# Kernel tuning notes

Hardware: AMD Instinct MI355X
Metric: run time of the kernel (lower is better)

## Reference

```python
import jax, jax.numpy as jnp
import numpy as np

H = 32        # num heads
D = 80        # head dim
HID = 2560    # hidden size = H*D
ROT = 32      # rotary dim = int(0.4*80)
THETA = 10000.0
T = 2048      # total packed tokens
B = 4         # sequences
SEQ = 512     # tokens per sequence
CACHE = 4096  # paged cache slots


def setup_inputs() -> dict:
    key = jax.random.key(0)
    ks = jax.random.split(key, 10)
    bound = 1.0 / np.sqrt(HID)

    def lin(k):
        kw, kb = jax.random.split(k)
        W = jax.random.uniform(kw, (HID, HID), jnp.float32, -bound, bound)
        b = jax.random.uniform(kb, (HID,), jnp.float32, -bound, bound)
        return W, b

    Wq, bq = lin(ks[0])
    Wk, bk = lin(ks[1])
    Wv, bv = lin(ks[2])
    Wd, bd = lin(ks[3])
    h = jax.random.normal(ks[4], (T, HID), jnp.float32)
    return {
        "h": h,
        "k_cache": jnp.zeros((CACHE, HID), jnp.float32),
        "v_cache": jnp.zeros((CACHE, HID), jnp.float32),
        "positions": (jnp.arange(T) % SEQ).astype(jnp.int32),
        "offsets": (jnp.arange(B + 1) * SEQ).astype(jnp.int32),
        "cache_indices": jnp.arange(T, dtype=jnp.int32),
        "Wq": Wq, "bq": bq, "Wk": Wk, "bk": bk,
        "Wv": Wv, "bv": bv, "Wd": Wd, "bd": bd,
    }


def _rotate_half(x):
    x1, x2 = jnp.split(x, 2, axis=-1)
    return jnp.concatenate([-x2, x1], axis=-1)


def reference(h, k_cache, v_cache, positions, offsets, cache_indices,
              Wq, bq, Wk, bk, Wv, bv, Wd, bd):
    # QKV projections (torch Linear: x @ W.T + b)
    q = h @ Wq.T + bq
    k = h @ Wk.T + bk
    v = h @ Wv.T + bv

    q3 = q.reshape(T, H, D)
    k3 = k.reshape(T, H, D)

    # partial RoPE on first ROT dims of each head
    pos = positions.astype(jnp.float32)
    inv_freq = 1.0 / (THETA ** (jnp.arange(0, ROT, 2, dtype=jnp.float32) / ROT))
    freqs = pos[:, None] * inv_freq                      # [T, ROT/2]
    emb = jnp.concatenate([freqs, freqs], axis=-1)       # [T, ROT]
    cos = jnp.cos(emb)[:, None, :]                       # [T, 1, ROT]
    sin = jnp.sin(emb)[:, None, :]

    q_rot, q_pass = q3[..., :ROT], q3[..., ROT:]
    k_rot, k_pass = k3[..., :ROT], k3[..., ROT:]
    q_rot = q_rot * cos + _rotate_half(q_rot) * sin
    k_rot = k_rot * cos + _rotate_half(k_rot) * sin
    q3 = jnp.concatenate([q_rot, q_pass], axis=-1)
    k3 = jnp.concatenate([k_rot, k_pass], axis=-1)

    # prompt_init=True path: scatter rotated k and v into paged caches
    new_k_cache = k_cache.at[cache_indices].set(k3.reshape(T, HID))
    new_v_cache = v_cache.at[cache_indices].set(v)

    # variable-length causal attention over packed sequences
    scale = D ** -0.5
    scores = jnp.einsum('thd,shd->hts', q3, k3) * scale   # [H, T, T]
    idx = jnp.arange(T)
    seg = jnp.searchsorted(offsets[1:], idx, side='right')
    mask = (seg[:, None] == seg[None, :]) & (idx[:, None] >= idx[None, :])
    scores = jnp.where(mask[None], scores, jnp.float32(-1e30))
    p = jax.nn.softmax(scores, axis=-1)
    o = jnp.einsum('hts,shd->thd', p, v.reshape(T, H, D)).reshape(T, HID)

    out = o @ Wd.T + bd
    return out, new_k_cache, new_v_cache
```

## Files before the change

kernel.cpp:

```cpp
#include <hip/hip_runtime.h>
#include <cstdint>
#include <cstddef>


#define HIDDEN 2560
#define SEQT 2048
#define NHEADS 32
#define DHEAD 80
#define NSEG 4
#define SEGLEN 512
#define CACHE_ROWS 4096
#define QSCALE 0.11180339887498949f

typedef __bf16 bf16_8 __attribute__((ext_vector_type(8)));
typedef unsigned short u16x8 __attribute__((ext_vector_type(8)));
typedef float f32x4 __attribute__((ext_vector_type(4)));

__device__ __forceinline__ unsigned short f2bf(float f) {
  unsigned int u = __builtin_bit_cast(unsigned int, f);
  u += 0x7fffu + ((u >> 16) & 1u);
  return (unsigned short)(u >> 16);
}
__device__ __forceinline__ float bf2f(unsigned short s) {
  unsigned int u = ((unsigned int)s) << 16;
  return __builtin_bit_cast(float, u);
}

__device__ __forceinline__ void gload16(const unsigned short* g, unsigned short* l) {
  __builtin_amdgcn_global_load_lds(
      (const __attribute__((address_space(1))) unsigned int*)g,
      (__attribute__((address_space(3))) unsigned int*)l, 16, 0, 0);
}

#define BAR() asm volatile("s_barrier" ::: "memory")
#define LGKM0()                                          \
  do {                                                   \
    asm volatile("s_waitcnt lgkmcnt(0)" ::: "memory");   \
    __builtin_amdgcn_sched_barrier(0);                   \
  } while (0)
#define PRIO(x) __builtin_amdgcn_s_setprio(x)
#define MF(af, bf, c) c = __builtin_amdgcn_mfma_f32_16x16x32_bf16(af, bf, c, 0, 0, 0)

__global__ __launch_bounds__(256) void prep_kernel(
    const float* __restrict__ s0, const float* __restrict__ s1,
    const float* __restrict__ s2, const float* __restrict__ s3,
    const float* __restrict__ s4,
    const float* __restrict__ kci, const float* __restrict__ vci,
    unsigned short* __restrict__ d0, unsigned short* __restrict__ d1,
    unsigned short* __restrict__ d2, unsigned short* __restrict__ d3,
    unsigned short* __restrict__ d4,
    float* __restrict__ kco, float* __restrict__ vco) {
  const int z = blockIdx.z;
  const int stride = gridDim.x * blockDim.x;
  int i = blockIdx.x * blockDim.x + threadIdx.x;
  if (z < 5) {
    const float* s = z == 0 ? s0 : z == 1 ? s1 : z == 2 ? s2 : z == 3 ? s3 : s4;
    unsigned short* d = z == 0 ? d0 : z == 1 ? d1 : z == 2 ? d2 : z == 3 ? d3 : d4;
    const int n4 = (z < 4) ? (HIDDEN * HIDDEN / 4) : (SEQT * HIDDEN / 4);
    for (; i < n4; i += stride) {
      float4 v = ((const float4*)s)[i];
      ushort4 o;
      o.x = f2bf(v.x); o.y = f2bf(v.y); o.z = f2bf(v.z); o.w = f2bf(v.w);
      ((ushort4*)d)[i] = o;
    }
  } else {
    const int n4 = SEQT * HIDDEN / 4;
    const float4* s = (const float4*)(z == 5 ? kci : vci);
    float4* d = (float4*)(z == 5 ? kco : vco);
    for (; i < n4; i += stride) d[i + n4] = s[i + n4];
  }
}

template <int OUTMODE>
__device__ __forceinline__ void gemm256_body(
    const unsigned short* __restrict__ A, const unsigned short* __restrict__ Bg,
    const float* __restrict__ bias, void* __restrict__ C,
    int m0, int n0, int kbase, int nt) {
  constexpr int K = HIDDEN;
  __shared__ __align__(16) unsigned short L[65536];

  const int tid = threadIdx.x;
  const int lane = tid & 63;
  const int wid = tid >> 6;
  const int l15 = lane & 15;
  const int kg = lane >> 4;
  const int wm = wid >> 2;
  const int wn = wid & 3;

  const int g8 = (((tid & 7) - (tid >> 3)) & 7) * 8;
  const int srow = tid >> 3;
  const unsigned short* As0 = A + (size_t)(m0 + srow) * K + kbase + g8;
  const unsigned short* As1 = As0 + (size_t)128 * K;
  const unsigned short* Bs0 = Bg + (size_t)(n0 + srow) * K + kbase + g8;
  const unsigned short* Bs1 = Bs0 + (size_t)128 * K;
  const int t16 = tid * 8;

  auto stA0 = [&](int kt) {
    const int b = (kt & 1) * 32768, ko = kt * 64;
    gload16(As0 + ko, L + b + t16);
    gload16(As1 + ko, L + b + 8192 + t16);
  };
  auto stA1 = [&](int kt) {
    const int b = (kt & 1) * 32768, ko = 64 * K + kt * 64;
    gload16(As0 + ko, L + b + 4096 + t16);
    gload16(As1 + ko, L + b + 12288 + t16);
  };
  auto stB0 = [&](int kt) {
    const int b = (kt & 1) * 32768 + 16384, ko = kt * 64;
    gload16(Bs0 + ko, L + b + t16);
    gload16(Bs0 + 64 * K + ko, L + b + 4096 + t16);
  };
  auto stB1 = [&](int kt) {
    const int b = (kt & 1) * 32768 + 16384 + 8192, ko = kt * 64;
    gload16(Bs1 + ko, L + b + t16);
    gload16(Bs1 + 64 * K + ko, L + b + 4096 + t16);
  };

  const int c0 = (kg + l15) & 7;
  const int aof0 = wm * 8192 + l15 * 64 + c0 * 8;
  const int aof1 = wm * 8192 + l15 * 64 + (c0 ^ 4) * 8;
  const int bof0 = 16384 + wn * 4096 + l15 * 64 + c0 * 8;
  const int bof1 = 16384 + wn * 4096 + l15 * 64 + (c0 ^ 4) * 8;

  f32x4 acc[8][4];
#pragma unroll
  for (int m = 0; m < 8; m++)
#pragma unroll
    for (int n = 0; n < 4; n++) acc[m][n] = f32x4{0.f, 0.f, 0.f, 0.f};

  bf16_8 a[4][2], bl[2][2], bh[2][2];

#define DSR(off) (*(const bf16_8*)(L + (off)))
  auto rdA = [&](int off) {
#pragma unroll
    for (int fm = 0; fm < 4; fm++) {
      a[fm][0] = DSR(off + aof0 + fm * 1024);
      a[fm][1] = DSR(off + aof1 + fm * 1024);
    }
  };
  auto rdBl = [&](int off) {
#pragma unroll
    for (int fn = 0; fn < 2; fn++) {
      bl[fn][0] = DSR(off + bof0 + fn * 1024);
      bl[fn][1] = DSR(off + bof1 + fn * 1024);
    }
  };
  auto rdBh = [&](int off) {
#pragma unroll
    for (int fn = 0; fn < 2; fn++) {
      bh[fn][0] = DSR(off + bof0 + (2 + fn) * 1024);
      bh[fn][1] = DSR(off + bof1 + (2 + fn) * 1024);
    }
  };
  auto mmq = [&](int mq, int nq, bf16_8 (&bb)[2][2]) {
#pragma unroll
    for (int fm = 0; fm < 4; fm++)
#pragma unroll
      for (int fn = 0; fn < 2; fn++) {
        MF(a[fm][0], bb[fn][0], acc[mq * 4 + fm][nq * 2 + fn]);
        MF(a[fm][1], bb[fn][1], acc[mq * 4 + fm][nq * 2 + fn]);
      }
  };

  stA0(0); stB0(0); stB1(0); stA1(0);
  stA0(1); stB0(1); stB1(1);
  asm volatile("s_waitcnt vmcnt(6)" ::: "memory");
  BAR();

#pragma unroll 2
  for (int t = 0; t < nt - 2; ++t) {
    const int bo = (t & 1) * 32768;
    rdA(bo); rdBl(bo);
    stA1(t + 1);
    BAR(); LGKM0(); PRIO(1); mmq(0, 0, bl); PRIO(0); BAR();
    rdBh(bo);
    stA0(t + 2);
    BAR(); LGKM0(); PRIO(1); mmq(0, 1, bh); PRIO(0); BAR();
    rdA(bo + 4096);
    stB0(t + 2);
    BAR(); LGKM0(); PRIO(1); mmq(1, 0, bl); PRIO(0); BAR();
    stB1(t + 2);
    BAR(); PRIO(1); mmq(1, 1, bh); PRIO(0);
    asm volatile("s_waitcnt vmcnt(6)" ::: "memory");
    BAR();
  }

  {
    const int bo = 0;
    rdA(bo); rdBl(bo);
    stA1(nt - 1);
    BAR(); LGKM0(); PRIO(1); mmq(0, 0, bl); PRIO(0); BAR();
    rdBh(bo);
    BAR(); LGKM0(); PRIO(1); mmq(0, 1, bh); PRIO(0); BAR();
    rdA(bo + 4096);
    BAR(); LGKM0(); PRIO(1); mmq(1, 0, bl); PRIO(0); BAR();
    BAR(); PRIO(1); mmq(1, 1, bh); PRIO(0);
    asm volatile("s_waitcnt vmcnt(0)" ::: "memory");
    BAR();
  }
  {
    const int bo = 32768;
    rdA(bo); rdBl(bo);
    BAR(); LGKM0(); PRIO(1); mmq(0, 0, bl); PRIO(0); BAR();
    rdBh(bo);
    BAR(); LGKM0(); PRIO(1); mmq(0, 1, bh); PRIO(0); BAR();
    rdA(bo + 4096);
    BAR(); LGKM0(); PRIO(1); mmq(1, 0, bl); PRIO(0); BAR();
    PRIO(1); mmq(1, 1, bh); PRIO(0);
  }
#undef DSR

#pragma unroll
  for (int n4 = 0; n4 < 4; n4++) {
    const int col = n0 + wn * 64 + n4 * 16 + l15;
    const float bv = (OUTMODE == 2) ? 0.f : bias[col];
#pragma unroll
    for (int m8 = 0; m8 < 8; m8++) {
      const int rowb = m0 + wm * 128 + m8 * 16 + kg * 4;
#pragma unroll
      for (int j = 0; j < 4; j++) {
        float val = acc[m8][n4][j] + bv;
        if (OUTMODE == 0)
          ((unsigned short*)C)[(size_t)(rowb + j) * HIDDEN + col] = f2bf(val);
        else
          ((float*)C)[(size_t)(rowb + j) * HIDDEN + col] = val;
      }
    }
  }
}

__global__ __launch_bounds__(512, 2) void gemm_qkv8_kernel(
    const unsigned short* __restrict__ A,
    const unsigned short* __restrict__ B0, const unsigned short* __restrict__ B1,
    const unsigned short* __restrict__ B2,
    const float* __restrict__ bias0, const float* __restrict__ bias1,
    const float* __restrict__ bias2,
    unsigned short* __restrict__ C0, unsigned short* __restrict__ C1,
    unsigned short* __restrict__ C2) {
  const int lb = blockIdx.x + 8 * (blockIdx.y + 10 * blockIdx.z);
  const int swz = (lb & 7) * 30 + (lb >> 3);
  const int mx = swz & 7;
  const int r = swz >> 3;
  const int ny = r % 10;
  const int zz = r / 10;
  const unsigned short* B = zz == 0 ? B0 : (zz == 1 ? B1 : B2);
  const float* bias = zz == 0 ? bias0 : (zz == 1 ? bias1 : bias2);
  unsigned short* C = zz == 0 ? C0 : (zz == 1 ? C1 : C2);
  gemm256_body<0>(A, B, bias, C, mx * 256, ny * 256, 0, 40);
}

__global__ __launch_bounds__(512, 2) void gemm_out8_kernel(
    const unsigned short* __restrict__ A, const unsigned short* __restrict__ B,
    float* __restrict__ P0, float* __restrict__ P1, float* __restrict__ P2) {
  const int lb = blockIdx.x + 8 * (blockIdx.y + 10 * blockIdx.z);
  const int swz = (lb & 7) * 30 + (lb >> 3);
  const int mx = swz & 7;
  const int r = swz >> 3;
  const int ny = r % 10;
  const int kz = r / 10;
  float* P = kz == 0 ? P0 : (kz == 1 ? P1 : P2);
  const int kbase = kz * 896;
  const int nt = (kz == 2) ? 12 : 14;
  gemm256_body<2>(A, B, nullptr, P, mx * 256, ny * 256, kbase, nt);
}

__global__ __launch_bounds__(256) void reduce3_bias_kernel(
    const float* __restrict__ p0, const float* __restrict__ p1,
    const float* __restrict__ p2, const float* __restrict__ bias,
    float* __restrict__ out, int n4) {
  int i = blockIdx.x * blockDim.x + threadIdx.x;
  const int stride = gridDim.x * blockDim.x;
  for (; i < n4; i += stride) {
    float4 a = ((const float4*)p0)[i];
    float4 b = ((const float4*)p1)[i];
    float4 c = ((const float4*)p2)[i];
    const int cb = (i * 4) % HIDDEN;
    float4 bv = *(const float4*)&bias[cb];
    float4 o;
    o.x = a.x + b.x + c.x + bv.x;
    o.y = a.y + b.y + c.y + bv.y;
    o.z = a.z + b.z + c.z + bv.z;
    o.w = a.w + b.w + c.w + bv.w;
    ((float4*)out)[i] = o;
  }
}

__global__ __launch_bounds__(256) void rope_scatter_kernel(
    unsigned short* __restrict__ qb, unsigned short* __restrict__ kb,
    const unsigned short* __restrict__ vb,
    const int* __restrict__ positions, const int* __restrict__ cidx,
    float* __restrict__ kco, float* __restrict__ vco) {
  const int t = blockIdx.x;
  const int tid = threadIdx.x;
  __shared__ float cs[16], sn[16];

  if (tid < 16) {
    const float pos = (float)positions[t];
    const float inv = expf(-(float)tid * (9.210340371976184f / 16.0f));
    const float f = pos * inv;
    cs[tid] = cosf(f);
    sn[tid] = sinf(f);
  }
  __syncthreads();

  {
    unsigned short* buf = (tid >> 7) ? kb : qb;
    const int r = tid & 127;
    const int head = r >> 2;
    const int d0 = (r & 3) * 4;
    unsigned short* p = buf + (size_t)t * HIDDEN + head * DHEAD + d0;
    ushort4 u1 = *(const ushort4*)p;
    ushort4 u2 = *(const ushort4*)(p + 16);
    ushort4 o1, o2;
#pragma unroll
    for (int e = 0; e < 4; e++) {
      const float c = cs[d0 + e], s = sn[d0 + e];
      const float x1 = bf2f((&u1.x)[e]);
      const float x2 = bf2f((&u2.x)[e]);
      (&o1.x)[e] = f2bf(x1 * c - x2 * s);
      (&o2.x)[e] = f2bf(x2 * c + x1 * s);
    }
    *(ushort4*)p = o1;
    *(ushort4*)(p + 16) = o2;
  }
  __syncthreads();

  const int ci = cidx[t];
  float* krow = kco + (size_t)ci * HIDDEN;
  float* vrow = vco + (size_t)ci * HIDDEN;
  const unsigned short* ks = kb + (size_t)t * HIDDEN;
  const unsigned short* vs = vb + (size_t)t * HIDDEN;
  for (int j = tid; j < 2 * (HIDDEN / 4); j += 256) {
    const int w = j >= (HIDDEN / 4);
    const int e4 = j - w * (HIDDEN / 4);
    const unsigned short* src = (w ? vs : ks) + e4 * 4;
    float* dst = (w ? vrow : krow) + e4 * 4;
    ushort4 u = *(const ushort4*)src;
    float4 f;
    f.x = bf2f(u.x); f.y = bf2f(u.y); f.z = bf2f(u.z); f.w = bf2f(u.w);
    *(float4*)dst = f;
  }
}

#define KSTR 104
#define VSTR 72
#define PSTR 72

__global__ __launch_bounds__(256) void attn_mfma_kernel(
    const unsigned short* __restrict__ qb, const unsigned short* __restrict__ kb,
    const unsigned short* __restrict__ vb, unsigned short* __restrict__ ob) {
  const int qt = blockIdx.x;
  const int h = blockIdx.y;
  const int seg = blockIdx.z;
  const int tq0 = seg * SEGLEN + qt * 64;

  __shared__ unsigned short Kt[64 * KSTR];
  __shared__ unsigned short VtT[80 * VSTR];
  __shared__ unsigned short Pw[4][16 * PSTR];

  const int tid = threadIdx.x;
  const int lane = tid & 63;
  const int w = tid >> 6;
  const int l15 = lane & 15;
  const int g = lane >> 4;

  bf16_8 qa[3];
  {
    const unsigned short* qp = qb + (size_t)(tq0 + w * 16 + l15) * HIDDEN + h * DHEAD;
#pragma unroll
    for (int c = 0; c < 3; c++) {
      u16x8 t = (u16x8)(unsigned short)0;
      const int d0 = c * 32 + g * 8;
      if (d0 < DHEAD) {
#pragma unroll
        for (int e = 0; e < 8; e++) t[e] = f2bf(bf2f(qp[d0 + e]) * QSCALE);
      }
      qa[c] = __builtin_bit_cast(bf16_8, t);
    }
  }

  float m_[4], l_[4];
#pragma unroll
  for (int j = 0; j < 4; j++) { m_[j] = -3.0e38f; l_[j] = 0.f; }
  f32x4 Oacc[5];
#pragma unroll
  for (int n = 0; n < 5; n++) Oacc[n] = f32x4{0.f, 0.f, 0.f, 0.f};

  for (int st = 0; st <= qt; ++st) {
    const int ts0 = seg * SEGLEN + st * 64;
    __syncthreads();
    for (int i = tid; i < 64 * 20; i += 256) {
      const int row = i / 20;
      const int c = i - row * 20;
      const size_t gsrc = (size_t)(ts0 + row) * HIDDEN + h * DHEAD + c * 4;
      ushort4 kv = *(const ushort4*)(kb + gsrc);
      ushort4 vv = *(const ushort4*)(vb + gsrc);
      *(ushort4*)&Kt[row * KSTR + c * 4] = kv;
      VtT[(c * 4 + 0) * VSTR + row] = vv.x;
      VtT[(c * 4 + 1) * VSTR + row] = vv.y;
      VtT[(c * 4 + 2) * VSTR + row] = vv.z;
      VtT[(c * 4 + 3) * VSTR + row] = vv.w;
    }
    __syncthreads();

    f32x4 Sacc[4];
#pragma unroll
    for (int t = 0; t < 4; t++) Sacc[t] = f32x4{0.f, 0.f, 0.f, 0.f};
#pragma unroll
    for (int c = 0; c < 3; c++) {
#pragma unroll
      for (int t = 0; t < 4; t++) {
        bf16_8 kf;
        if (c < 2 || g < 2)
          kf = *(const bf16_8*)&Kt[(t * 16 + l15) * KSTR + c * 32 + g * 8];
        else
          kf = __builtin_bit_cast(bf16_8, (u16x8)(unsigned short)0);
        Sacc[t] = __builtin_amdgcn_mfma_f32_16x16x32_bf16(qa[c], kf, Sacc[t], 0, 0, 0);
      }
    }

    if (st == qt) {
#pragma unroll
      for (int t = 0; t < 4; t++)
#pragma unroll
        for (int j = 0; j < 4; j++)
          if (t * 16 + l15 > w * 16 + 4 * g + j) Sacc[t][j] = -1e30f;
    }

    float pm[4], ps[4], rold[4];
#pragma unroll
    for (int j = 0; j < 4; j++)
      pm[j] = fmaxf(fmaxf(Sacc[0][j], Sacc[1][j]), fmaxf(Sacc[2][j], Sacc[3][j]));
#pragma unroll
    for (int d = 1; d < 16; d <<= 1)
#pragma unroll
      for (int j = 0; j < 4; j++) pm[j] = fmaxf(pm[j], __shfl_xor(pm[j], d, 64));
#pragma unroll
    for (int j = 0; j < 4; j++) {
      const float mn = fmaxf(m_[j], pm[j]);
      rold[j] = __expf(m_[j] - mn);
      m_[j] = mn;
      ps[j] = 0.f;
    }
#pragma unroll
    for (int t = 0; t < 4; t++)
#pragma unroll
      for (int j = 0; j < 4; j++) {
        const float p = __expf(Sacc[t][j] - m_[j]);
        Sacc[t][j] = p;
        ps[j] += p;
      }
#pragma unroll
    for (int d = 1; d < 16; d <<= 1)
#pragma unroll
      for (int j = 0; j < 4; j++) ps[j] += __shfl_xor(ps[j], d, 64);
#pragma unroll
    for (int j = 0; j < 4; j++) l_[j] = l_[j] * rold[j] + ps[j];

#pragma unroll
    for (int t = 0; t < 4; t++)
#pragma unroll
      for (int j = 0; j < 4; j++)
        Pw[w][(4 * g + j) * PSTR + t * 16 + l15] = f2bf(Sacc[t][j]);
#pragma unroll
    for (int n = 0; n < 5; n++)
#pragma unroll
      for (int j = 0; j < 4; j++) Oacc[n][j] *= rold[j];

#pragma unroll
    for (int c = 0; c < 2; c++) {
      bf16_8 pa = *(const bf16_8*)&Pw[w][l15 * PSTR + c * 32 + g * 8];
#pragma unroll
      for (int n = 0; n < 5; n++) {
        bf16_8 vf = *(const bf16_8*)&VtT[(n * 16 + l15) * VSTR + c * 32 + g * 8];
        Oacc[n] = __builtin_amdgcn_mfma_f32_16x16x32_bf16(pa, vf, Oacc[n], 0, 0, 0);
      }
    }
  }

  float inv[4];
#pragma unroll
  for (int j = 0; j < 4; j++) inv[j] = 1.f / l_[j];
  unsigned short* op = ob + (size_t)(tq0 + w * 16) * HIDDEN + h * DHEAD;
#pragma unroll
  for (int n = 0; n < 5; n++)
#pragma unroll
    for (int j = 0; j < 4; j++)
      op[(size_t)(4 * g + j) * HIDDEN + n * 16 + l15] = f2bf(Oacc[n][j] * inv[j]);
}

extern "C" void kernel_launch(void* const* d_in, const int* in_sizes, int n_in,
                              void* d_out, int out_size, void* d_ws, size_t ws_size,
                              hipStream_t stream) {
  const float* h = (const float*)d_in[0];
  const float* kci = (const float*)d_in[1];
  const float* vci = (const float*)d_in[2];
  const int* positions = (const int*)d_in[3];
  const int* cidx = (const int*)d_in[5];
  const float* Wq = (const float*)d_in[6];
  const float* bq = (const float*)d_in[7];
  const float* Wk = (const float*)d_in[8];
  const float* bk = (const float*)d_in[9];
  const float* Wv = (const float*)d_in[10];
  const float* bv = (const float*)d_in[11];
  const float* Wd = (const float*)d_in[12];
  const float* bd = (const float*)d_in[13];

  float* out = (float*)d_out;
  float* kco = out + (size_t)SEQT * HIDDEN;
  float* vco = kco + (size_t)CACHE_ROWS * HIDDEN;

  char* ws = (char*)d_ws;
  char* ws0 = ws;
  unsigned short* h_bf = (unsigned short*)ws;  ws += (size_t)SEQT * HIDDEN * 2;
  unsigned short* Wq_bf = (unsigned short*)ws; ws += (size_t)HIDDEN * HIDDEN * 2;
  unsigned short* Wk_bf = (unsigned short*)ws; ws += (size_t)HIDDEN * HIDDEN * 2;
  unsigned short* Wv_bf = (unsigned short*)ws; ws += (size_t)HIDDEN * HIDDEN * 2;
  unsigned short* Wd_bf = (unsigned short*)ws; ws += (size_t)HIDDEN * HIDDEN * 2;
  unsigned short* q_bf = (unsigned short*)ws;  ws += (size_t)SEQT * HIDDEN * 2;
  unsigned short* k_bf = (unsigned short*)ws;  ws += (size_t)SEQT * HIDDEN * 2;
  unsigned short* v_bf = (unsigned short*)ws;  ws += (size_t)SEQT * HIDDEN * 2;
  unsigned short* o_bf = (unsigned short*)ws;  ws += (size_t)SEQT * HIDDEN * 2;

  float* part0 = (float*)ws0;
  float* part1 = part0 + (size_t)SEQT * HIDDEN;
  float* part2 = (float*)q_bf;

  {
    dim3 gp(2048, 1, 7);
    prep_kernel<<<gp, 256, 0, stream>>>(Wq, Wk, Wv, Wd, h, kci, vci,
                                        Wq_bf, Wk_bf, Wv_bf, Wd_bf, h_bf,
                                        kco, vco);
  }

  {
    dim3 gq(SEQT / 256, HIDDEN / 256, 3);
    gemm_qkv8_kernel<<<gq, 512, 0, stream>>>(h_bf, Wq_bf, Wk_bf, Wv_bf, bq, bk, bv,
                                             q_bf, k_bf, v_bf);
  }

  rope_scatter_kernel<<<SEQT, 256, 0, stream>>>(q_bf, k_bf, v_bf, positions, cidx, kco, vco);

  {
    dim3 ga(SEGLEN / 64, NHEADS, NSEG);
    attn_mfma_kernel<<<ga, 256, 0, stream>>>(q_bf, k_bf, v_bf, o_bf);
  }

  {
    dim3 go(SEQT / 256, HIDDEN / 256, 3);
    gemm_out8_kernel<<<go, 512, 0, stream>>>(o_bf, Wd_bf, part0, part1, part2);
  }
  reduce3_bias_kernel<<<2048, 256, 0, stream>>>(part0, part1, part2, bd, out,
                                                SEQT * HIDDEN / 4);
}
```

Measured before the change: 246.6 us.

## Fuse V-cache scatter into QKV GEMM epilogue and drop explicit LDS waits

Writes the fp32 V values directly into the paged V cache from the QKV GEMM epilogue, so the rope/scatter kernel only handles K. Removes the explicit lgkmcnt(0) waits and scheduling barriers before each MFMA quarter in the GEMM loop, leaving wait placement to the compiler. Vectorizes the Q fragment load in attention. Risks include uncoalesced scalar cache stores in the epilogue and possible LDS read hazards if compiler waits are insufficient.

```diff
diff --git a/kernel.cpp b/kernel.cpp
--- a/kernel.cpp
+++ b/kernel.cpp
@@ -33,11 +33,6 @@
 }
 
 #define BAR() asm volatile("s_barrier" ::: "memory")
-#define LGKM0()                                          \
-  do {                                                   \
-    asm volatile("s_waitcnt lgkmcnt(0)" ::: "memory");   \
-    __builtin_amdgcn_sched_barrier(0);                   \
-  } while (0)
 #define PRIO(x) __builtin_amdgcn_s_setprio(x)
 #define MF(af, bf, c) c = __builtin_amdgcn_mfma_f32_16x16x32_bf16(af, bf, c, 0, 0, 0)
 
@@ -75,7 +70,8 @@
 __device__ __forceinline__ void gemm256_body(
     const unsigned short* __restrict__ A, const unsigned short* __restrict__ Bg,
     const float* __restrict__ bias, void* __restrict__ C,
-    int m0, int n0, int kbase, int nt) {
+    int m0, int n0, int kbase, int nt,
+    const int* __restrict__ cidx, float* __restrict__ vcache) {
   constexpr int K = HIDDEN;
   __shared__ __align__(16) unsigned short L[65536];
 
@@ -172,13 +168,13 @@
     const int bo = (t & 1) * 32768;
     rdA(bo); rdBl(bo);
     stA1(t + 1);
-    BAR(); LGKM0(); PRIO(1); mmq(0, 0, bl); PRIO(0); BAR();
+    BAR(); PRIO(1); mmq(0, 0, bl); PRIO(0); BAR();
     rdBh(bo);
     stA0(t + 2);
-    BAR(); LGKM0(); PRIO(1); mmq(0, 1, bh); PRIO(0); BAR();
+    BAR(); PRIO(1); mmq(0, 1, bh); PRIO(0); BAR();
     rdA(bo + 4096);
     stB0(t + 2);
-    BAR(); LGKM0(); PRIO(1); mmq(1, 0, bl); PRIO(0); BAR();
+    BAR(); PRIO(1); mmq(1, 0, bl); PRIO(0); BAR();
     stB1(t + 2);
     BAR(); PRIO(1); mmq(1, 1, bh); PRIO(0);
     asm volatile("s_waitcnt vmcnt(6)" ::: "memory");
@@ -189,11 +185,11 @@
     const int bo = 0;
     rdA(bo); rdBl(bo);
     stA1(nt - 1);
-    BAR(); LGKM0(); PRIO(1); mmq(0, 0, bl); PRIO(0); BAR();
+    BAR(); PRIO(1); mmq(0, 0, bl); PRIO(0); BAR();
     rdBh(bo);
-    BAR(); LGKM0(); PRIO(1); mmq(0, 1, bh); PRIO(0); BAR();
+    BAR(); PRIO(1); mmq(0, 1, bh); PRIO(0); BAR();
     rdA(bo + 4096);
-    BAR(); LGKM0(); PRIO(1); mmq(1, 0, bl); PRIO(0); BAR();
+    BAR(); PRIO(1); mmq(1, 0, bl); PRIO(0); BAR();
     BAR(); PRIO(1); mmq(1, 1, bh); PRIO(0);
     asm volatile("s_waitcnt vmcnt(0)" ::: "memory");
     BAR();
@@ -201,11 +197,11 @@
   {
     const int bo = 32768;
     rdA(bo); rdBl(bo);
-    BAR(); LGKM0(); PRIO(1); mmq(0, 0, bl); PRIO(0); BAR();
+    BAR(); PRIO(1); mmq(0, 0, bl); PRIO(0); BAR();
     rdBh(bo);
-    BAR(); LGKM0(); PRIO(1); mmq(0, 1, bh); PRIO(0); BAR();
+    BAR(); PRIO(1); mmq(0, 1, bh); PRIO(0); BAR();
     rdA(bo + 4096);
-    BAR(); LGKM0(); PRIO(1); mmq(1, 0, bl); PRIO(0); BAR();
+    BAR(); PRIO(1); mmq(1, 0, bl); PRIO(0); BAR();
     PRIO(1); mmq(1, 1, bh); PRIO(0);
   }
 #undef DSR
@@ -220,10 +216,13 @@
 #pragma unroll
       for (int j = 0; j < 4; j++) {
         float val = acc[m8][n4][j] + bv;
-        if (OUTMODE == 0)
+        if (OUTMODE == 0) {
           ((unsigned short*)C)[(size_t)(rowb + j) * HIDDEN + col] = f2bf(val);
-        else
+          if (vcache != nullptr)
+            vcache[(size_t)cidx[rowb + j] * HIDDEN + col] = val;
+        } else {
           ((float*)C)[(size_t)(rowb + j) * HIDDEN + col] = val;
+        }
       }
     }
   }
@@ -236,7 +235,8 @@
     const float* __restrict__ bias0, const float* __restrict__ bias1,
     const float* __restrict__ bias2,
     unsigned short* __restrict__ C0, unsigned short* __restrict__ C1,
-    unsigned short* __restrict__ C2) {
+    unsigned short* __restrict__ C2,
+    const int* __restrict__ cidx, float* __restrict__ vco) {
   const int lb = blockIdx.x + 8 * (blockIdx.y + 10 * blockIdx.z);
   const int swz = (lb & 7) * 30 + (lb >> 3);
   const int mx = swz & 7;
@@ -246,7 +246,8 @@
   const unsigned short* B = zz == 0 ? B0 : (zz == 1 ? B1 : B2);
   const float* bias = zz == 0 ? bias0 : (zz == 1 ? bias1 : bias2);
   unsigned short* C = zz == 0 ? C0 : (zz == 1 ? C1 : C2);
-  gemm256_body<0>(A, B, bias, C, mx * 256, ny * 256, 0, 40);
+  float* vcache = (zz == 2) ? vco : nullptr;
+  gemm256_body<0>(A, B, bias, C, mx * 256, ny * 256, 0, 40, cidx, vcache);
 }
 
 __global__ __launch_bounds__(512, 2) void gemm_out8_kernel(
@@ -261,7 +262,7 @@
   float* P = kz == 0 ? P0 : (kz == 1 ? P1 : P2);
   const int kbase = kz * 896;
   const int nt = (kz == 2) ? 12 : 14;
-  gemm256_body<2>(A, B, nullptr, P, mx * 256, ny * 256, kbase, nt);
+  gemm256_body<2>(A, B, nullptr, P, mx * 256, ny * 256, kbase, nt, nullptr, nullptr);
 }
 
 __global__ __launch_bounds__(256) void reduce3_bias_kernel(
@@ -287,9 +288,8 @@
 
 __global__ __launch_bounds__(256) void rope_scatter_kernel(
     unsigned short* __restrict__ qb, unsigned short* __restrict__ kb,
-    const unsigned short* __restrict__ vb,
     const int* __restrict__ positions, const int* __restrict__ cidx,
-    float* __restrict__ kco, float* __restrict__ vco) {
+    float* __restrict__ kco) {
   const int t = blockIdx.x;
   const int tid = threadIdx.x;
   __shared__ float cs[16], sn[16];
@@ -327,18 +327,12 @@
 
   const int ci = cidx[t];
   float* krow = kco + (size_t)ci * HIDDEN;
-  float* vrow = vco + (size_t)ci * HIDDEN;
   const unsigned short* ks = kb + (size_t)t * HIDDEN;
-  const unsigned short* vs = vb + (size_t)t * HIDDEN;
-  for (int j = tid; j < 2 * (HIDDEN / 4); j += 256) {
-    const int w = j >= (HIDDEN / 4);
-    const int e4 = j - w * (HIDDEN / 4);
-    const unsigned short* src = (w ? vs : ks) + e4 * 4;
-    float* dst = (w ? vrow : krow) + e4 * 4;
-    ushort4 u = *(const ushort4*)src;
+  for (int j = tid; j < HIDDEN / 4; j += 256) {
+    ushort4 u = *(const ushort4*)(ks + j * 4);
     float4 f;
     f.x = bf2f(u.x); f.y = bf2f(u.y); f.z = bf2f(u.z); f.w = bf2f(u.w);
-    *(float4*)dst = f;
+    *(float4*)(krow + j * 4) = f;
   }
 }
 
@@ -372,8 +366,12 @@
       u16x8 t = (u16x8)(unsigned short)0;
       const int d0 = c * 32 + g * 8;
       if (d0 < DHEAD) {
-#pragma unroll
-        for (int e = 0; e < 8; e++) t[e] = f2bf(bf2f(qp[d0 + e]) * QSCALE);
+        ushort4 v0 = *(const ushort4*)(qp + d0);
+        ushort4 v1 = *(const ushort4*)(qp + d0 + 4);
+        t[0] = f2bf(bf2f(v0.x) * QSCALE); t[1] = f2bf(bf2f(v0.y) * QSCALE);
+        t[2] = f2bf(bf2f(v0.z) * QSCALE); t[3] = f2bf(bf2f(v0.w) * QSCALE);
+        t[4] = f2bf(bf2f(v1.x) * QSCALE); t[5] = f2bf(bf2f(v1.y) * QSCALE);
+        t[6] = f2bf(bf2f(v1.z) * QSCALE); t[7] = f2bf(bf2f(v1.w) * QSCALE);
       }
       qa[c] = __builtin_bit_cast(bf16_8, t);
     }
@@ -536,10 +534,10 @@
   {
     dim3 gq(SEQT / 256, HIDDEN / 256, 3);
     gemm_qkv8_kernel<<<gq, 512, 0, stream>>>(h_bf, Wq_bf, Wk_bf, Wv_bf, bq, bk, bv,
-                                             q_bf, k_bf, v_bf);
-  }
-
-  rope_scatter_kernel<<<SEQT, 256, 0, stream>>>(q_bf, k_bf, v_bf, positions, cidx, kco, vco);
+                                             q_bf, k_bf, v_bf, cidx, vco);
+  }
+
+  rope_scatter_kernel<<<SEQT, 256, 0, stream>>>(q_bf, k_bf, positions, cidx, kco);
 
   {
     dim3 ga(SEGLEN / 64, NHEADS, NSEG);
```

Measured after the change: 256.3 us. +3.9%, slower.
